# Kernel tuning notes

Hardware: AMD Instinct MI355X
Metric: run time of the kernel (lower is better)

Reference implementation:

```python
import jax, jax.numpy as jnp
import numpy as np

N, M, FIN, K, OUT, E = 8, 49152, 64, 6, 64, 393216


def setup_inputs() -> dict:
    key = jax.random.key(0)
    k1, k2, k3, k4, k5, k6 = jax.random.split(key, 6)
    x = jax.random.normal(k1, (N, M, FIN), jnp.float32)
    rows = jax.random.randint(k2, (E,), 0, M, jnp.int32)
    cols = jax.random.randint(k3, (E,), 0, M, jnp.int32)
    vals = jax.random.normal(k4, (E,), jnp.float32) * 0.1  # scaled-Laplacian values
    stdv = 1.0 / np.sqrt(OUT)
    weight = jax.random.uniform(k5, (FIN * K, OUT), jnp.float32, -stdv, stdv)
    bias = jax.random.uniform(k6, (OUT,), jnp.float32, -stdv, stdv)
    return {"x": x, "rows": rows, "cols": cols, "vals": vals,
            "weight": weight, "bias": bias}


def reference(x, rows, cols, vals, weight, bias):
    # x: [N, M, Fin]; L sparse [M, M] in COO (rows, cols, vals)
    n, m, fin = x.shape
    # x0: [M, Fin*N] as in torch permute(1,2,0).view(M, Fin*N)
    x0 = jnp.transpose(x, (1, 2, 0)).reshape(m, fin * n)

    def spmm(X):  # L @ X via gather + segment-sum scatter
        return jax.ops.segment_sum(vals[:, None] * X[cols], rows, num_segments=m)

    xs = [x0]
    if K > 1:
        x1 = spmm(x0)
        xs.append(x1)
        for _ in range(2, K):
            x2 = 2.0 * spmm(x1) - x0
            xs.append(x2)
            x0, x1 = x1, x2

    # stack -> [K, M, Fin, N]; torch then permutes to [N, M, Fin, K] and
    # flattens to (N*M, Fin*K) with Fin outer, K inner: weight row idx = f*K + k
    T = jnp.stack(xs, 0).reshape(K, m, fin, n)
    Wr = weight.reshape(fin, K, OUT)
    out = jnp.einsum('kmfn,fko->nmo', T, Wr) + bias  # [N, M, OUT]
    return jax.nn.elu(out)
```

## Files before the change

### kernel.cpp

```cpp
#include <hip/hip_runtime.h>
#include <hip/hip_bf16.h>
#include <math.h>

#define N_    8
#define M_    49152
#define FIN_  64
#define K_    6
#define OUT_  64
#define E_    393216
#define ROW_  512

typedef __attribute__((ext_vector_type(8))) short bf16x8;
typedef __attribute__((ext_vector_type(4))) float f32x4;

static __device__ __forceinline__ unsigned short f2bf(float f) {
    unsigned u = __float_as_uint(f);
    u += 0x7fff + ((u >> 16) & 1);
    return (unsigned short)(u >> 16);
}
static __device__ __forceinline__ float bfl(unsigned u) { return __uint_as_float(u << 16); }
static __device__ __forceinline__ float bfh(unsigned u) { return __uint_as_float(u & 0xffff0000u); }


__global__ void count_kernel(const int* __restrict__ rows, int* __restrict__ cnt) {
    int e = blockIdx.x * blockDim.x + threadIdx.x;
    if (e < E_) atomicAdd(&cnt[rows[e]], 1);
}

__global__ __launch_bounds__(1024) void scan_kernel(int* __restrict__ cntfill, int* __restrict__ rowptr) {
    __shared__ int lws[768];
    __shared__ int lw2[12];
    int t = threadIdx.x;
    int lane = t & 63, wid = t >> 6;
    int v[48], d[48];
    #pragma unroll
    for (int ch = 0; ch < 48; ++ch) v[ch] = cntfill[ch * 1024 + t];
    #pragma unroll
    for (int ch = 0; ch < 48; ++ch) {
        int s = v[ch];
        #pragma unroll
        for (int off = 1; off < 64; off <<= 1) {
            int y = __shfl_up(s, off, 64);
            if (lane >= off) s += y;
        }
        d[ch] = s - v[ch];
        if (lane == 63) lws[ch * 16 + wid] = s;
    }
    __syncthreads();
    int orig = 0, s2 = 0;
    if (t < 768) {
        orig = lws[t];
        s2 = orig;
        #pragma unroll
        for (int off = 1; off < 64; off <<= 1) {
            int y = __shfl_up(s2, off, 64);
            if (lane >= off) s2 += y;
        }
        if (lane == 63) lw2[t >> 6] = s2;
    }
    __syncthreads();
    if (t == 0) {
        int run = 0;
        #pragma unroll
        for (int i = 0; i < 12; ++i) { int c = lw2[i]; lw2[i] = run; run += c; }
    }
    __syncthreads();
    if (t < 768) lws[t] = lw2[t >> 6] + s2 - orig;
    __syncthreads();
    #pragma unroll
    for (int ch = 0; ch < 48; ++ch) {
        int excl = lws[ch * 16 + wid] + d[ch];
        rowptr[ch * 1024 + t]  = excl;
        cntfill[ch * 1024 + t] = excl;
    }
    if (t == 0) rowptr[M_] = E_;
}

__global__ void fill_kernel(const int* __restrict__ rows, const int* __restrict__ cols,
                            const float* __restrict__ vals, int* __restrict__ fillpos,
                            int* __restrict__ ecol, float* __restrict__ evalv,
                            int* __restrict__ eidx) {
    int e = blockIdx.x * blockDim.x + threadIdx.x;
    if (e < E_) {
        int r = rows[e];
        int p = atomicAdd(&fillpos[r], 1);
        ecol[p]  = cols[e];
        evalv[p] = vals[e];
        eidx[p]  = e;
    }
}

__global__ void sort_kernel(const int* __restrict__ rowptr, int* __restrict__ ecol,
                            float* __restrict__ evalv, int* __restrict__ eidx) {
    int m = blockIdx.x * blockDim.x + threadIdx.x;
    if (m >= M_) return;
    int s = rowptr[m], e = rowptr[m + 1];
    for (int i = s + 1; i < e; ++i) {
        int ki = eidx[i]; int kc = ecol[i]; float kv = evalv[i];
        int j = i - 1;
        while (j >= s && eidx[j] > ki) {
            eidx[j + 1] = eidx[j]; ecol[j + 1] = ecol[j]; evalv[j + 1] = evalv[j];
            --j;
        }
        eidx[j + 1] = ki; ecol[j + 1] = kc; evalv[j + 1] = kv;
    }
}


__global__ void permute_count_kernel(const float* __restrict__ x, unsigned short* __restrict__ T0,
                                     const int* __restrict__ rows, int* __restrict__ cnt) {
    int idx = blockIdx.x * blockDim.x + threadIdx.x;
    int f4 = idx & 15, n = (idx >> 4) & 7, m = idx >> 7;
    float4 v = ((const float4*)x)[(size_t)(n * M_ + m) * 16 + f4];
    ushort4 o;
    o.x = f2bf(v.x); o.y = f2bf(v.y); o.z = f2bf(v.z); o.w = f2bf(v.w);
    *(ushort4*)(T0 + (size_t)m * ROW_ + n * 64 + f4 * 4) = o;
    if (idx < E_) atomicAdd(&cnt[rows[idx]], 1);
}

__global__ void fill_wprep_kernel(const int* __restrict__ rows, const int* __restrict__ cols,
                                  const float* __restrict__ vals, int* __restrict__ fillpos,
                                  int* __restrict__ ecol, float* __restrict__ evalv,
                                  int* __restrict__ eidx,
                                  const float* __restrict__ W, unsigned short* __restrict__ Wfrag) {
    int e = blockIdx.x * blockDim.x + threadIdx.x;
    if (e < E_) {
        int r = rows[e];
        int p = atomicAdd(&fillpos[r], 1);
        ecol[p]  = cols[e];
        evalv[p] = vals[e];
        eidx[p]  = e;
    }
    if (e < 24576) {
        int i = e & 7, l = (e >> 3) & 63, tile = (e >> 9) & 3, kk = e >> 11;
        int kcheb = kk >> 1;
        int f = (kk & 1) * 32 + (l >> 4) * 8 + i;
        int o = tile * 16 + (l & 15);
        Wfrag[e] = f2bf(W[(f * K_ + kcheb) * OUT_ + o]);
    }
}

static __device__ __forceinline__ void fma_u4(float* acc, float v, uint4 u) {
    acc[0] += v * bfl(u.x); acc[1] += v * bfh(u.x);
    acc[2] += v * bfl(u.y); acc[3] += v * bfh(u.y);
    acc[4] += v * bfl(u.z); acc[5] += v * bfh(u.z);
    acc[6] += v * bfl(u.w); acc[7] += v * bfh(u.w);
}

__global__ __launch_bounds__(256) void spmm_bf16_kernel(
        const unsigned short* __restrict__ cur, const unsigned short* __restrict__ prev,
        unsigned short* __restrict__ nxt,
        const int* __restrict__ rowptr, const int* __restrict__ ecol,
        const float* __restrict__ evalv, float alpha, float beta) {
    int t = threadIdx.x;
    int w = t >> 6, l = t & 63;
    int m = blockIdx.x * 4 + w;
    int s = rowptr[m], e = rowptr[m + 1];
    int cnt = e - s;
    int myc = 0; float myv = 0.f;
    if (l < cnt) { myc = ecol[s + l]; myv = evalv[s + l]; }
    uint4 p;
    if (beta != 0.f) p = *(const uint4*)(prev + (size_t)m * ROW_ + l * 8);

    float acc[8] = {0.f, 0.f, 0.f, 0.f, 0.f, 0.f, 0.f, 0.f};
    int lim = cnt < 64 ? cnt : 64;
    int i = 0;
    for (; i + 3 < lim; i += 4) {
        int c0 = __shfl(myc, i),     c1 = __shfl(myc, i + 1);
        int c2 = __shfl(myc, i + 2), c3 = __shfl(myc, i + 3);
        float v0 = __shfl(myv, i),     v1 = __shfl(myv, i + 1);
        float v2 = __shfl(myv, i + 2), v3 = __shfl(myv, i + 3);
        uint4 u0 = *(const uint4*)(cur + (size_t)c0 * ROW_ + l * 8);
        uint4 u1 = *(const uint4*)(cur + (size_t)c1 * ROW_ + l * 8);
        uint4 u2 = *(const uint4*)(cur + (size_t)c2 * ROW_ + l * 8);
        uint4 u3 = *(const uint4*)(cur + (size_t)c3 * ROW_ + l * 8);
        fma_u4(acc, v0, u0); fma_u4(acc, v1, u1);
        fma_u4(acc, v2, u2); fma_u4(acc, v3, u3);
    }
    for (; i < lim; ++i) {
        int c0 = __shfl(myc, i);
        float v0 = __shfl(myv, i);
        uint4 u0 = *(const uint4*)(cur + (size_t)c0 * ROW_ + l * 8);
        fma_u4(acc, v0, u0);
    }
    for (int j = 64; j < cnt; ++j) {
        int c0 = ecol[s + j];
        float v0 = evalv[s + j];
        uint4 u0 = *(const uint4*)(cur + (size_t)c0 * ROW_ + l * 8);
        fma_u4(acc, v0, u0);
    }
    #pragma unroll
    for (int j = 0; j < 8; ++j) acc[j] *= alpha;
    if (beta != 0.f) {
        acc[0] += beta * bfl(p.x); acc[1] += beta * bfh(p.x);
        acc[2] += beta * bfl(p.y); acc[3] += beta * bfh(p.y);
        acc[4] += beta * bfl(p.z); acc[5] += beta * bfh(p.z);
        acc[6] += beta * bfl(p.w); acc[7] += beta * bfh(p.w);
    }
    uint4 o;
    o.x = (unsigned)f2bf(acc[0]) | ((unsigned)f2bf(acc[1]) << 16);
    o.y = (unsigned)f2bf(acc[2]) | ((unsigned)f2bf(acc[3]) << 16);
    o.z = (unsigned)f2bf(acc[4]) | ((unsigned)f2bf(acc[5]) << 16);
    o.w = (unsigned)f2bf(acc[6]) | ((unsigned)f2bf(acc[7]) << 16);
    *(uint4*)(nxt + (size_t)m * ROW_ + l * 8) = o;
}

static __device__ __forceinline__ void epilogue_tile(
        f32x4 acc, int tile, int rbase, int col, float b,
        float* __restrict__ outn) {
    int c = tile * 16 + col;
    #pragma unroll
    for (int v = 0; v < 4; ++v) {
        float r = acc[v] + b;
        r = r > 0.f ? r : (__expf(r) - 1.f);
        outn[(size_t)(rbase + v) * OUT_ + c] = r;
    }
}

__global__ __launch_bounds__(256) void combine_kernel(
        const unsigned short* __restrict__ Tbase,
        const unsigned short* __restrict__ Wfrag,
        const float* __restrict__ bias, float* __restrict__ out) {
    __shared__ unsigned short wlds[24576];
    int t = threadIdx.x;
    {
        const uint4* src = (const uint4*)Wfrag;
        uint4* dst = (uint4*)wlds;
        #pragma unroll
        for (int i = 0; i < 12; ++i)
            dst[t + 256 * i] = src[t + 256 * i];
    }
    __syncthreads();

    int w = t >> 6, l = t & 63;
    int m0 = blockIdx.x * 64 + w * 16;
    int arow = m0 + (l & 15);
    const size_t MROW = (size_t)M_ * ROW_;
    size_t abase0 = (size_t)arow * ROW_ + (l >> 4) * 8;
    int rbase = m0 + (l >> 4) * 4;
    int col = l & 15;
    float b0 = bias[col], b1 = bias[16 + col], b2 = bias[32 + col], b3 = bias[48 + col];

    #pragma unroll
    for (int n = 0; n < 8; ++n) {
        size_t abase = abase0 + n * 64;
        bf16x8 a[12];
        #pragma unroll
        for (int kk = 0; kk < 12; ++kk)
            a[kk] = *(const bf16x8*)(Tbase + (size_t)(kk >> 1) * MROW + abase + (kk & 1) * 32);

        f32x4 acc0 = {0.f, 0.f, 0.f, 0.f};
        f32x4 acc1 = {0.f, 0.f, 0.f, 0.f};
        f32x4 acc2 = {0.f, 0.f, 0.f, 0.f};
        f32x4 acc3 = {0.f, 0.f, 0.f, 0.f};
        #pragma unroll
        for (int kk = 0; kk < 12; ++kk) {
            const unsigned short* wp = wlds + ((size_t)(kk * 4) * 64 + l) * 8;
            bf16x8 q0 = *(const bf16x8*)(wp);
            bf16x8 q1 = *(const bf16x8*)(wp + 512);
            bf16x8 q2 = *(const bf16x8*)(wp + 1024);
            bf16x8 q3 = *(const bf16x8*)(wp + 1536);
            acc0 = __builtin_amdgcn_mfma_f32_16x16x32_bf16(a[kk], q0, acc0, 0, 0, 0);
            acc1 = __builtin_amdgcn_mfma_f32_16x16x32_bf16(a[kk], q1, acc1, 0, 0, 0);
            acc2 = __builtin_amdgcn_mfma_f32_16x16x32_bf16(a[kk], q2, acc2, 0, 0, 0);
            acc3 = __builtin_amdgcn_mfma_f32_16x16x32_bf16(a[kk], q3, acc3, 0, 0, 0);
        }

        float* outn = out + (size_t)n * ((size_t)M_ * OUT_);
        epilogue_tile(acc0, 0, rbase, col, b0, outn);
        epilogue_tile(acc1, 1, rbase, col, b1, outn);
        epilogue_tile(acc2, 2, rbase, col, b2, outn);
        epilogue_tile(acc3, 3, rbase, col, b3, outn);
    }
}


__global__ void permute_kernel(const float* __restrict__ x, float* __restrict__ A) {
    int idx = blockIdx.x * blockDim.x + threadIdx.x;
    int f4 = idx & 15;
    int n  = (idx >> 4) & 7;
    int m  = idx >> 7;
    float4 v = ((const float4*)x)[(size_t)(n * M_ + m) * 16 + f4];
    ((float4*)A)[idx] = v;
}

__global__ __launch_bounds__(512) void step_kernel(
        const float* __restrict__ cur, float* __restrict__ nxt,
        const float* __restrict__ weight, const float* __restrict__ bias,
        const int* __restrict__ rowptr, const int* __restrict__ ecol,
        const float* __restrict__ evalv, float* __restrict__ out,
        int k, float alpha, float beta, int flags) {
    __shared__ float lds_x[ROW_];
    int m = blockIdx.x;
    int t = threadIdx.x;
    lds_x[t] = cur[(size_t)m * ROW_ + t];
    if (flags & 4) {
        float acc = 0.f;
        int s = rowptr[m], e = rowptr[m + 1];
        for (int i = s; i < e; ++i)
            acc += evalv[i] * cur[(size_t)ecol[i] * ROW_ + t];
        float prevv = (beta != 0.f) ? nxt[(size_t)m * ROW_ + t] : 0.f;
        nxt[(size_t)m * ROW_ + t] = alpha * acc + beta * prevv;
    }
    __syncthreads();
    int n = t >> 6, o = t & 63;
    const float4* lx4 = (const float4*)(lds_x + n * FIN_);
    float acc = 0.f;
    #pragma unroll
    for (int f4 = 0; f4 < 16; ++f4) {
        float4 xq = lx4[f4];
        int fb = f4 * 4;
        acc += xq.x * weight[((fb + 0) * K_ + k) * OUT_ + o];
        acc += xq.y * weight[((fb + 1) * K_ + k) * OUT_ + o];
        acc += xq.z * weight[((fb + 2) * K_ + k) * OUT_ + o];
        acc += xq.w * weight[((fb + 3) * K_ + k) * OUT_ + o];
    }
    size_t oidx = (size_t)n * (M_ * OUT_) + (size_t)m * OUT_ + o;
    float res = (flags & 1) ? acc : (out[oidx] + acc);
    if (flags & 2) {
        res += bias[o];
        res = (res > 0.f) ? res : (expf(res) - 1.f);
    }
    out[oidx] = res;
}


extern "C" void kernel_launch(void* const* d_in, const int* in_sizes, int n_in,
                              void* d_out, int out_size, void* d_ws, size_t ws_size,
                              hipStream_t stream) {
    (void)in_sizes; (void)n_in; (void)out_size;
    const float* x      = (const float*)d_in[0];
    const int*   rows   = (const int*)d_in[1];
    const int*   cols   = (const int*)d_in[2];
    const float* vals   = (const float*)d_in[3];
    const float* weight = (const float*)d_in[4];
    const float* bias   = (const float*)d_in[5];
    float* out = (float*)d_out;

    char* ws = (char*)d_ws;
    size_t off = 0;
    auto alloc = [&](size_t bytes) -> void* {
        void* p = ws + off;
        off += (bytes + 255) & ~(size_t)255;
        return p;
    };

    const size_t tbytes = (size_t)M_ * ROW_ * 2;
    const size_t need_new = 6 * (tbytes + 256) + (M_ + 1) * 4 + M_ * 4
                          + 3 * ((size_t)E_ * 4 + 256) + 24576 * 2 + 4096;

    if (ws_size >= need_new) {
        unsigned short* T[6];
        for (int i = 0; i < 6; ++i) T[i] = (unsigned short*)alloc(tbytes);
        int*   rowptr  = (int*)alloc((size_t)(M_ + 1) * 4);
        int*   fillpos = (int*)alloc((size_t)M_ * 4);
        int*   ecol    = (int*)alloc((size_t)E_ * 4);
        float* evalv   = (float*)alloc((size_t)E_ * 4);
        int*   eidx    = (int*)alloc((size_t)E_ * 4);
        unsigned short* Wfrag = (unsigned short*)alloc(24576 * 2);

        hipMemsetAsync(fillpos, 0, (size_t)M_ * 4, stream);
        permute_count_kernel<<<(M_ * N_ * 16) / 256, 256, 0, stream>>>(x, T[0], rows, fillpos);
        scan_kernel<<<1, 1024, 0, stream>>>(fillpos, rowptr);
        fill_wprep_kernel<<<E_ / 256, 256, 0, stream>>>(rows, cols, vals, fillpos,
                                                        ecol, evalv, eidx, weight, Wfrag);
        sort_kernel<<<M_ / 256, 256, 0, stream>>>(rowptr, ecol, evalv, eidx);

        spmm_bf16_kernel<<<M_ / 4, 256, 0, stream>>>(T[0], T[0], T[1], rowptr, ecol, evalv, 1.f, 0.f);
        spmm_bf16_kernel<<<M_ / 4, 256, 0, stream>>>(T[1], T[0], T[2], rowptr, ecol, evalv, 2.f, -1.f);
        spmm_bf16_kernel<<<M_ / 4, 256, 0, stream>>>(T[2], T[1], T[3], rowptr, ecol, evalv, 2.f, -1.f);
        spmm_bf16_kernel<<<M_ / 4, 256, 0, stream>>>(T[3], T[2], T[4], rowptr, ecol, evalv, 2.f, -1.f);
        spmm_bf16_kernel<<<M_ / 4, 256, 0, stream>>>(T[4], T[3], T[5], rowptr, ecol, evalv, 2.f, -1.f);

        combine_kernel<<<M_ / 64, 256, 0, stream>>>(T[0], Wfrag, bias, out);
    } else {
        float* A       = (float*)alloc((size_t)M_ * ROW_ * 4);
        float* B       = (float*)alloc((size_t)M_ * ROW_ * 4);
        int*   rowptr  = (int*)alloc((size_t)(M_ + 1) * 4);
        int*   fillpos = (int*)alloc((size_t)M_ * 4);
        int*   ecol    = (int*)alloc((size_t)E_ * 4);
        float* evalv   = (float*)alloc((size_t)E_ * 4);
        int*   eidx    = (int*)alloc((size_t)E_ * 4);

        permute_kernel<<<(M_ * N_ * 16) / 256, 256, 0, stream>>>(x, A);
        hipMemsetAsync(fillpos, 0, (size_t)M_ * 4, stream);
        count_kernel<<<E_ / 256, 256, 0, stream>>>(rows, fillpos);
        scan_kernel<<<1, 1024, 0, stream>>>(fillpos, rowptr);
        fill_kernel<<<E_ / 256, 256, 0, stream>>>(rows, cols, vals, fillpos, ecol, evalv, eidx);
        sort_kernel<<<M_ / 256, 256, 0, stream>>>(rowptr, ecol, evalv, eidx);

        step_kernel<<<M_, 512, 0, stream>>>(A, B, weight, bias, rowptr, ecol, evalv, out, 0, 1.f, 0.f, 1 | 4);
        step_kernel<<<M_, 512, 0, stream>>>(B, A, weight, bias, rowptr, ecol, evalv, out, 1, 2.f, -1.f, 4);
        step_kernel<<<M_, 512, 0, stream>>>(A, B, weight, bias, rowptr, ecol, evalv, out, 2, 2.f, -1.f, 4);
        step_kernel<<<M_, 512, 0, stream>>>(B, A, weight, bias, rowptr, ecol, evalv, out, 3, 2.f, -1.f, 4);
        step_kernel<<<M_, 512, 0, stream>>>(A, B, weight, bias, rowptr, ecol, evalv, out, 4, 2.f, -1.f, 4);
        step_kernel<<<M_, 512, 0, stream>>>(B, B, weight, bias, rowptr, ecol, evalv, out, 5, 0.f, 0.f, 2);
    }
}
```

Measured before the change: 639.9 us.

## Split single-block scan into three-phase multi-block scan; enlarge combine blocks

Replaces the single-workgroup exclusive scan over row counts with a three-kernel scan: per-block local scans across 48 blocks, a tiny scan of the block sums, then an add-offset pass. This removes a serial single-CU bottleneck at the cost of two extra launches. The combine kernel also moves to 512-thread blocks covering 128 rows each, which halves the per-block weight staging into LDS relative to the rows processed.

```diff
diff --git a/kernel.cpp b/kernel.cpp
--- a/kernel.cpp
+++ b/kernel.cpp
@@ -27,53 +27,51 @@
     if (e < E_) atomicAdd(&cnt[rows[e]], 1);
 }
 
-__global__ __launch_bounds__(1024) void scan_kernel(int* __restrict__ cntfill, int* __restrict__ rowptr) {
-    __shared__ int lws[768];
-    __shared__ int lw2[12];
-    int t = threadIdx.x;
-    int lane = t & 63, wid = t >> 6;
-    int v[48], d[48];
-    #pragma unroll
-    for (int ch = 0; ch < 48; ++ch) v[ch] = cntfill[ch * 1024 + t];
-    #pragma unroll
-    for (int ch = 0; ch < 48; ++ch) {
-        int s = v[ch];
-        #pragma unroll
-        for (int off = 1; off < 64; off <<= 1) {
-            int y = __shfl_up(s, off, 64);
-            if (lane >= off) s += y;
-        }
-        d[ch] = s - v[ch];
-        if (lane == 63) lws[ch * 16 + wid] = s;
-    }
-    __syncthreads();
-    int orig = 0, s2 = 0;
-    if (t < 768) {
-        orig = lws[t];
-        s2 = orig;
-        #pragma unroll
-        for (int off = 1; off < 64; off <<= 1) {
-            int y = __shfl_up(s2, off, 64);
-            if (lane >= off) s2 += y;
-        }
-        if (lane == 63) lw2[t >> 6] = s2;
-    }
+__global__ __launch_bounds__(1024) void scanA_kernel(const int* __restrict__ cnt,
+                                                     int* __restrict__ lscan,
+                                                     int* __restrict__ bsum) {
+    __shared__ int wsum[16];
+    int b = blockIdx.x, t = threadIdx.x, lane = t & 63, wid = t >> 6;
+    int v = cnt[b * 1024 + t];
+    int s = v;
+    #pragma unroll
+    for (int off = 1; off < 64; off <<= 1) {
+        int y = __shfl_up(s, off, 64);
+        if (lane >= off) s += y;
+    }
+    if (lane == 63) wsum[wid] = s;
     __syncthreads();
     if (t == 0) {
         int run = 0;
         #pragma unroll
-        for (int i = 0; i < 12; ++i) { int c = lw2[i]; lw2[i] = run; run += c; }
+        for (int i = 0; i < 16; ++i) { int c = wsum[i]; wsum[i] = run; run += c; }
+        bsum[b] = run;
     }
     __syncthreads();
-    if (t < 768) lws[t] = lw2[t >> 6] + s2 - orig;
-    __syncthreads();
-    #pragma unroll
-    for (int ch = 0; ch < 48; ++ch) {
-        int excl = lws[ch * 16 + wid] + d[ch];
-        rowptr[ch * 1024 + t]  = excl;
-        cntfill[ch * 1024 + t] = excl;
-    }
+    lscan[b * 1024 + t] = wsum[wid] + s - v;
+}
+
+__global__ void scanB_kernel(const int* __restrict__ bsum, int* __restrict__ boffs,
+                             int* __restrict__ rowptr) {
+    int t = threadIdx.x;
+    int v = (t < 48) ? bsum[t] : 0;
+    int s = v;
+    #pragma unroll
+    for (int off = 1; off < 64; off <<= 1) {
+        int y = __shfl_up(s, off, 64);
+        if (t >= off) s += y;
+    }
+    if (t < 48) boffs[t] = s - v;
     if (t == 0) rowptr[M_] = E_;
+}
+
+__global__ __launch_bounds__(1024) void scanC_kernel(int* __restrict__ rowptr,
+                                                     const int* __restrict__ boffs,
+                                                     int* __restrict__ cntfill) {
+    int b = blockIdx.x, t = threadIdx.x;
+    int val = rowptr[b * 1024 + t] + boffs[b];
+    rowptr[b * 1024 + t]  = val;
+    cntfill[b * 1024 + t] = val;
 }
 
 __global__ void fill_kernel(const int* __restrict__ rows, const int* __restrict__ cols,
@@ -217,7 +215,7 @@
     }
 }
 
-__global__ __launch_bounds__(256) void combine_kernel(
+__global__ __launch_bounds__(512) void combine_kernel(
         const unsigned short* __restrict__ Tbase,
         const unsigned short* __restrict__ Wfrag,
         const float* __restrict__ bias, float* __restrict__ out) {
@@ -227,13 +225,13 @@
         const uint4* src = (const uint4*)Wfrag;
         uint4* dst = (uint4*)wlds;
         #pragma unroll
-        for (int i = 0; i < 12; ++i)
-            dst[t + 256 * i] = src[t + 256 * i];
+        for (int i = 0; i < 6; ++i)
+            dst[t + 512 * i] = src[t + 512 * i];
     }
     __syncthreads();
 
     int w = t >> 6, l = t & 63;
-    int m0 = blockIdx.x * 64 + w * 16;
+    int m0 = blockIdx.x * 128 + w * 16;
     int arow = m0 + (l & 15);
     const size_t MROW = (size_t)M_ * ROW_;
     size_t abase0 = (size_t)arow * ROW_ + (l >> 4) * 8;
@@ -347,7 +345,7 @@
 
     const size_t tbytes = (size_t)M_ * ROW_ * 2;
     const size_t need_new = 6 * (tbytes + 256) + (M_ + 1) * 4 + M_ * 4
-                          + 3 * ((size_t)E_ * 4 + 256) + 24576 * 2 + 4096;
+                          + 3 * ((size_t)E_ * 4 + 256) + 24576 * 2 + 8192;
 
     if (ws_size >= need_new) {
         unsigned short* T[6];
@@ -358,10 +356,14 @@
         float* evalv   = (float*)alloc((size_t)E_ * 4);
         int*   eidx    = (int*)alloc((size_t)E_ * 4);
         unsigned short* Wfrag = (unsigned short*)alloc(24576 * 2);
+        int*   bsum    = (int*)alloc(48 * 4);
+        int*   boffs   = (int*)alloc(48 * 4);
 
         hipMemsetAsync(fillpos, 0, (size_t)M_ * 4, stream);
         permute_count_kernel<<<(M_ * N_ * 16) / 256, 256, 0, stream>>>(x, T[0], rows, fillpos);
-        scan_kernel<<<1, 1024, 0, stream>>>(fillpos, rowptr);
+        scanA_kernel<<<48, 1024, 0, stream>>>(fillpos, rowptr, bsum);
+        scanB_kernel<<<1, 64, 0, stream>>>(bsum, boffs, rowptr);
+        scanC_kernel<<<48, 1024, 0, stream>>>(rowptr, boffs, fillpos);
         fill_wprep_kernel<<<E_ / 256, 256, 0, stream>>>(rows, cols, vals, fillpos,
                                                         ecol, evalv, eidx, weight, Wfrag);
         sort_kernel<<<M_ / 256, 256, 0, stream>>>(rowptr, ecol, evalv, eidx);
@@ -372,7 +374,7 @@
         spmm_bf16_kernel<<<M_ / 4, 256, 0, stream>>>(T[3], T[2], T[4], rowptr, ecol, evalv, 2.f, -1.f);
         spmm_bf16_kernel<<<M_ / 4, 256, 0, stream>>>(T[4], T[3], T[5], rowptr, ecol, evalv, 2.f, -1.f);
 
-        combine_kernel<<<M_ / 64, 256, 0, stream>>>(T[0], Wfrag, bias, out);
+        combine_kernel<<<M_ / 128, 512, 0, stream>>>(T[0], Wfrag, bias, out);
     } else {
         float* A       = (float*)alloc((size_t)M_ * ROW_ * 4);
         float* B       = (float*)alloc((size_t)M_ * ROW_ * 4);
@@ -381,11 +383,15 @@
         int*   ecol    = (int*)alloc((size_t)E_ * 4);
         float* evalv   = (float*)alloc((size_t)E_ * 4);
         int*   eidx    = (int*)alloc((size_t)E_ * 4);
+        int*   bsum    = (int*)alloc(48 * 4);
+        int*   boffs   = (int*)alloc(48 * 4);
 
         permute_kernel<<<(M_ * N_ * 16) / 256, 256, 0, stream>>>(x, A);
         hipMemsetAsync(fillpos, 0, (size_t)M_ * 4, stream);
         count_kernel<<<E_ / 256, 256, 0, stream>>>(rows, fillpos);
-        scan_kernel<<<1, 1024, 0, stream>>>(fillpos, rowptr);
+        scanA_kernel<<<48, 1024, 0, stream>>>(fillpos, rowptr, bsum);
+        scanB_kernel<<<1, 64, 0, stream>>>(bsum, boffs, rowptr);
+        scanC_kernel<<<48, 1024, 0, stream>>>(rowptr, boffs, fillpos);
         fill_kernel<<<E_ / 256, 256, 0, stream>>>(rows, cols, vals, fillpos, ecol, evalv, eidx);
         sort_kernel<<<M_ / 256, 256, 0, stream>>>(rowptr, ecol, evalv, eidx);
 
```

Result: faster. 562.0 us (-12.2%).
